# Performance work log

Hardware: AMD Instinct MI355X
Metric: run time of the kernel (lower is better)

The kernel has to match this reference:

```python
import jax, jax.numpy as jnp
import numpy as np

# Constants from init_kwargs
DT = 0.01
NIV = 8          # energy_input_dim[1]
HID = 64         # hidden_dims[0]
FEAT = 501       # per-field microstructure feature length (501+501=1002)


def _lin(k, fin, fout):
    return jax.random.normal(k, (fin, fout), dtype=jnp.float32) / np.sqrt(fin)


def setup_inputs() -> dict:
    key = jax.random.key(0)
    ks = jax.random.split(key, 12)
    B, T = 8192, 512
    e = jax.random.normal(ks[0], (B, T, 1), dtype=jnp.float32) * 0.1
    e_dot = jax.random.normal(ks[1], (B, T, 1), dtype=jnp.float32) * 0.1
    # positive microstructure fields (code computes nu**-1 and E/nu**2)
    E = jax.random.uniform(ks[2], (B, FEAT), minval=0.5, maxval=2.0, dtype=jnp.float32)
    nu = jax.random.uniform(ks[3], (B, FEAT), minval=0.5, maxval=2.0, dtype=jnp.float32)
    return {
        "e": e, "e_dot": e_dot, "E": E, "nu": nu,
        # EnergyFunction.B : Linear(1002,64) -> ReLU -> Linear(64,niv)
        "Bw1": _lin(ks[4], 2 * FEAT, HID), "Bb1": jnp.zeros((HID,), jnp.float32),
        "Bw2": _lin(ks[5], HID, NIV), "Bb2": jnp.zeros((NIV,), jnp.float32),
        # InverseDissipationPotential.beta : Linear(1002,64)->Softplus->Linear(64,niv)->Softplus
        "bw1": _lin(ks[6], 2 * FEAT, HID), "bb1": jnp.zeros((HID,), jnp.float32),
        "bw2": _lin(ks[7], HID, NIV), "bb2": jnp.zeros((NIV,), jnp.float32),
    }


def reference(e, e_dot, E, nu, Bw1, Bb1, Bw2, Bb2, bw1, bb1, bw2, bb2):
    # --- microstructure encoder (TrueFeatures) ---
    nu_p = 1.0 / jnp.mean(1.0 / nu, axis=1, keepdims=True)                 # [B,1]
    E_p = jnp.mean(E / nu ** 2, axis=1, keepdims=True) * nu_p ** 2         # [B,1]
    m = jnp.concatenate([E, nu], axis=-1)                                  # [B,1002]

    # Time-invariant MLP coefficients (hoisted out of the time loop)
    Bm = jax.nn.relu(m @ Bw1 + Bb1) @ Bw2 + Bb2                            # [B,NIV]
    beta = jax.nn.softplus(jax.nn.softplus(m @ bw1 + bb1) @ bw2 + bb2)     # [B,NIV]
    Bsum = jnp.sum(Bm, axis=-1, keepdims=True)                             # [B,1]

    B_, niv = Bm.shape
    xi0 = jnp.zeros((B_, niv), dtype=e.dtype)

    def step(xi, inp):
        u, p = inp                                                          # [B,1],[B,1]
        # Analytic gradients of L = sum_{b,k} Bm_bk * (0.5*E' u^2 + 0.5*(u-xi_k)^2 + 0.5*sum_j xi_j^2)
        du = u - xi                                                         # [B,NIV]
        grad_u = Bsum * E_p * u + jnp.sum(Bm * du, axis=-1, keepdims=True)  # [B,1] (s_eq)
        grad_v = -Bm * du + Bsum * xi                                       # [B,NIV] (d)
        q = -grad_v
        # Analytic gradients of potential = -0.5*nu' p^2 + 0.5*sum(beta*q^2)
        grad_p = -nu_p * p                                                  # [B,1] (s_neq)
        grad_q = beta * q                                                   # [B,NIV] (kinetics)
        stress = grad_u - grad_p
        return xi + DT * grad_q, (stress, xi)

    xs = (jnp.swapaxes(e, 0, 1), jnp.swapaxes(e_dot, 0, 1))                 # [T,B,1]
    _, (stress_t, xi_t) = jax.lax.scan(step, xi0, xs)
    stress = jnp.swapaxes(stress_t, 0, 1)                                   # [B,T,1]
    xi = jnp.swapaxes(xi_t, 0, 1)                                           # [B,T,NIV]
    return stress, xi
```

## Files before the change

kernel.cpp:

```cpp
#include <hip/hip_runtime.h>
#include <hip/hip_bf16.h>

#define FEATN 501
#define KPAD 1024
#define MSTRIDE 1032
#define NB 8192
#define NT 512
#define DTC 0.01f

typedef __attribute__((ext_vector_type(8))) short short8;
typedef __attribute__((ext_vector_type(4))) short short4v;
typedef __attribute__((ext_vector_type(4))) float f32x4;

__device__ __forceinline__ float softplus_f(float x) {
    return fmaxf(x, 0.f) + log1pf(expf(-fabsf(x)));
}
__device__ __forceinline__ ushort f2bf(float x) {
    __hip_bfloat16 h = __float2bfloat16(x);
    return *reinterpret_cast<ushort*>(&h);
}
__device__ __forceinline__ void gl_lds16(const void* g, void* l) {
    __builtin_amdgcn_global_load_lds(
        (const __attribute__((address_space(1))) void*)g,
        (__attribute__((address_space(3))) void*)l, 16, 0, 0);
}
__device__ __forceinline__ float dpp_add(float x, const int ctrl) {
    int s = __builtin_bit_cast(int, x);
    int y;
    switch (ctrl) {
    case 0xB1:  y = __builtin_amdgcn_update_dpp(0, s, 0xB1, 0xf, 0xf, true); break;
    case 0x4E:  y = __builtin_amdgcn_update_dpp(0, s, 0x4E, 0xf, 0xf, true); break;
    default:    y = __builtin_amdgcn_update_dpp(0, s, 0x141, 0xf, 0xf, true); break;
    }
    return x + __builtin_bit_cast(float, y);
}

__global__ __launch_bounds__(256) void wtrans_kernel(
    const float* __restrict__ Bw1, const float* __restrict__ bw1,
    ushort* __restrict__ Wt) {
    const int h = blockIdx.x;
    const int lane = threadIdx.x & 63;
    const int wv = threadIdx.x >> 6;
    const float* W = (h < 64) ? Bw1 : bw1;
    const int col = h & 63;
    #pragma unroll
    for (int it = 0; it < 4; ++it) {
        const int k = it * 256 + wv * 64 + lane;
        const int ksrc = (k < FEATN) ? k
                       : (k >= 512 && k < 512 + FEATN) ? k - 11 : -1;
        const float v = (ksrc >= 0) ? W[(size_t)ksrc * 64 + col] : 0.f;
        Wt[(size_t)h * KPAD + k] = f2bf(v);
    }
}

__global__ __launch_bounds__(1024, 8) void enc_kernel(
    const float* __restrict__ E, const float* __restrict__ nu,
    const ushort* __restrict__ Wt,
    const float* __restrict__ Bb1, const float* __restrict__ bb1,
    const float* __restrict__ Bw2, const float* __restrict__ Bb2,
    const float* __restrict__ bw2, const float* __restrict__ bb2,
    float* __restrict__ xi) {
    __shared__ ushort Ml[16 * MSTRIDE];
    __shared__ float red[3][2048];
    __shared__ float hid[128][17];
    __shared__ float nups[16], Eps[16];

    const int tid = threadIdx.x;
    const int w = tid >> 6, lane = tid & 63;
    const int bb0 = blockIdx.x * 16;

    {
        const int bl = w;
        const size_t base = (size_t)(bb0 + bl) * FEATN;
        float s1 = 0.f, s2 = 0.f;
        #pragma unroll
        for (int it = 0; it < 2; ++it) {
            const int i0 = it * 256 + lane * 4;
            if (i0 + 3 < FEATN) {
                const float4 Ev = *(const float4*)(E + base + i0);
                const float4 nv = *(const float4*)(nu + base + i0);
                const float i0v = 1.0f / nv.x, i1v = 1.0f / nv.y;
                const float i2v = 1.0f / nv.z, i3v = 1.0f / nv.w;
                s1 += (i0v + i1v) + (i2v + i3v);
                s2 = fmaf(Ev.x, i0v * i0v, s2);
                s2 = fmaf(Ev.y, i1v * i1v, s2);
                s2 = fmaf(Ev.z, i2v * i2v, s2);
                s2 = fmaf(Ev.w, i3v * i3v, s2);
                short4v ep = {(short)f2bf(Ev.x), (short)f2bf(Ev.y),
                              (short)f2bf(Ev.z), (short)f2bf(Ev.w)};
                short4v np_ = {(short)f2bf(nv.x), (short)f2bf(nv.y),
                               (short)f2bf(nv.z), (short)f2bf(nv.w)};
                *(short4v*)&Ml[bl * MSTRIDE + i0] = ep;
                *(short4v*)&Ml[bl * MSTRIDE + 512 + i0] = np_;
            } else if (i0 < FEATN) {
                const float Ev = E[base + i0];
                const float nv = nu[base + i0];
                const float iv = 1.0f / nv;
                s1 += iv;
                s2 = fmaf(Ev, iv * iv, s2);
                Ml[bl * MSTRIDE + i0] = f2bf(Ev);
                Ml[bl * MSTRIDE + 512 + i0] = f2bf(nv);
            }
        }
        if (lane < 11) {
            Ml[bl * MSTRIDE + FEATN + lane] = 0;
            Ml[bl * MSTRIDE + 512 + FEATN + lane] = 0;
        }
        #pragma unroll
        for (int o = 32; o; o >>= 1) {
            s1 += __shfl_xor(s1, o);
            s2 += __shfl_xor(s2, o);
        }
        if (lane == 0) {
            const float np = (float)FEATN / s1;
            nups[bl] = np;
            Eps[bl] = (s2 / (float)FEATN) * np * np;
        }
    }
    __syncthreads();

    const int g = w & 3, q = w >> 2;
    const int r15 = lane & 15, kg = lane >> 4;
    const ushort* wp0 = Wt + (size_t)(g * 32 + r15) * KPAD + q * 256 + kg * 8;
    const ushort* wp1 = wp0 + 16 * KPAD;
    const int boff = r15 * MSTRIDE + q * 256 + kg * 8;

    f32x4 acc0 = {0.f, 0.f, 0.f, 0.f}, acc1 = acc0;
    #pragma unroll
    for (int s = 0; s < 8; ++s) {
        const int kb = s * 32;
        const short8 a0 = *(const short8*)(wp0 + kb);
        const short8 a1 = *(const short8*)(wp1 + kb);
        const short8 b = *(const short8*)&Ml[boff + kb];
        acc0 = __builtin_amdgcn_mfma_f32_16x16x32_bf16(a0, b, acc0, 0, 0, 0);
        acc1 = __builtin_amdgcn_mfma_f32_16x16x32_bf16(a1, b, acc1, 0, 0, 0);
    }

    if (q > 0) {
        *(f32x4*)&red[q - 1][(g * 64 + lane) * 8] = acc0;
        *(f32x4*)&red[q - 1][(g * 64 + lane) * 8 + 4] = acc1;
    }
    __syncthreads();
    if (q == 0) {
        #pragma unroll
        for (int p = 0; p < 3; ++p) {
            acc0 += *(const f32x4*)&red[p][(g * 64 + lane) * 8];
            acc1 += *(const f32x4*)&red[p][(g * 64 + lane) * 8 + 4];
        }
        #pragma unroll
        for (int t = 0; t < 2; ++t) {
            #pragma unroll
            for (int r = 0; r < 4; ++r) {
                const int h = g * 32 + t * 16 + kg * 4 + r;
                const float bias = (h < 64) ? Bb1[h] : bb1[h - 64];
                float v = (t ? acc1[r] : acc0[r]) + bias;
                v = (h < 64) ? fmaxf(v, 0.f) : softplus_f(v);
                hid[h][r15] = v;
            }
        }
    }
    __syncthreads();

    if (tid < 128) {
        const int bl = tid >> 3, k = tid & 7;
        float dB = 0.f, db = 0.f;
        #pragma unroll 8
        for (int h = 0; h < 64; ++h) {
            dB = fmaf(hid[h][bl], Bw2[h * 8 + k], dB);
            db = fmaf(hid[64 + h][bl], bw2[h * 8 + k], db);
        }
        const float Bm = dB + Bb2[k];
        const float be = softplus_f(db + bb2[k]);
        float Bs = Bm;
        Bs += __shfl_xor(Bs, 1);
        Bs += __shfl_xor(Bs, 2);
        Bs += __shfl_xor(Bs, 4);
        float* cb = xi + (size_t)(bb0 + bl) * 4096;
        cb[k] = 1.f - DTC * be * (Bm + Bs);
        cb[8 + k] = DTC * be * Bm;
        cb[16 + k] = Bm;
        if (k == 0) { cb[24] = Bs * Eps[bl]; cb[25] = nups[bl]; }
    }
}

__global__ __launch_bounds__(256) void time_kernel(
    const float* __restrict__ e, const float* __restrict__ ed,
    const float* coef, float* stress, float* xi_out) {
    __shared__ float els[4][512];
    __shared__ float pls[4][512];
    __shared__ float scr[4][256];
    const int wv = threadIdx.x >> 6;
    const int wid = (blockIdx.x << 2) + wv;
    const int lane = threadIdx.x & 63;
    const int j = lane >> 3, k = lane & 7;

    const float* eb = e + (size_t)wid * NT;
    const float* edb = ed + (size_t)wid * NT;
    gl_lds16(eb + lane * 4, &els[wv][0]);
    gl_lds16(eb + 256 + lane * 4, &els[wv][256]);
    gl_lds16(edb + lane * 4, &pls[wv][0]);
    gl_lds16(edb + 256 + lane * 4, &pls[wv][256]);

    const float* cb = coef + (size_t)wid * 4096;
    const float a = cb[k];
    const float c = cb[8 + k];
    const float Bm = cb[16 + k];
    const float sE = cb[24];
    const float nup = cb[25];
    asm volatile("s_waitcnt vmcnt(0)" ::: "memory");

    const float a2 = a * a, a4 = a2 * a2;
    float A = 1.f;
    if (j & 1) A *= a;
    if (j & 2) A *= a2;
    if (j & 4) A *= a4;
    float pw[8];
    {
        float run = c;
        #pragma unroll
        for (int i = 7; i >= 0; --i) {
            const bool on = (i < j);
            pw[i] = on ? run : 0.f;
            run = on ? run * a : run;
        }
    }

    float* xb = xi_out + (size_t)wid * (NT * 8);
    float* sb = stress + (size_t)wid * NT;
    const float* el = &els[wv][0];
    const float* pl = &pls[wv][0];

    float4 q0 = *(const float4*)(el);
    float4 q1 = *(const float4*)(el + 4);
    float uj = el[j];
    float pj = pl[j];

    float xs = 0.f;
    for (int g = 0; g < 16; ++g) {
        const int T0 = g * 32;
        float vx[4], sv[4];
        #pragma unroll
        for (int w = 0; w < 4; ++w) {
            const int t0 = T0 + w * 8;
            const float u0 = q0.x, u1 = q0.y, u2 = q0.z, u3 = q0.w;
            const float u4 = q1.x, u5 = q1.y, u6 = q1.z, u7 = q1.w;
            const float cuj = uj, cpj = pj;
            if (t0 + 8 < NT) {
                q0 = *(const float4*)(el + t0 + 8);
                q1 = *(const float4*)(el + t0 + 12);
                uj = el[t0 + 8 + j];
                pj = pl[t0 + 8 + j];
            }
            float xi_j = A * xs;
            xi_j = fmaf(pw[0], u0, xi_j);
            xi_j = fmaf(pw[1], u1, xi_j);
            xi_j = fmaf(pw[2], u2, xi_j);
            xi_j = fmaf(pw[3], u3, xi_j);
            xi_j = fmaf(pw[4], u4, xi_j);
            xi_j = fmaf(pw[5], u5, xi_j);
            xi_j = fmaf(pw[6], u6, xi_j);
            xi_j = fmaf(pw[7], u7, xi_j);
            vx[w] = xi_j;
            float r = Bm * (cuj - xi_j);
            r = dpp_add(r, 0xB1);
            r = dpp_add(r, 0x4E);
            r = dpp_add(r, 0x141);
            sv[w] = fmaf(sE, cuj, fmaf(nup, cpj, r));
            xs = fmaf(a, __shfl(xi_j, 56 + k), c * u7);
        }
        #pragma unroll
        for (int w = 0; w < 4; ++w) scr[wv][w * 64 + lane] = vx[w];
        *(float4*)(xb + T0 * 8 + lane * 4) =
            *(const float4*)&scr[wv][lane * 4];
        if (k == 0) {
            #pragma unroll
            for (int w = 0; w < 4; ++w) scr[wv][w * 8 + j] = sv[w];
        }
        if (lane < 8)
            *(float4*)(sb + T0 + lane * 4) =
                *(const float4*)&scr[wv][lane * 4];
    }
}

extern "C" void kernel_launch(void* const* d_in, const int* in_sizes, int n_in,
                              void* d_out, int out_size, void* d_ws, size_t ws_size,
                              hipStream_t stream) {
    const float* e   = (const float*)d_in[0];
    const float* ed  = (const float*)d_in[1];
    const float* E   = (const float*)d_in[2];
    const float* nu  = (const float*)d_in[3];
    const float* Bw1 = (const float*)d_in[4];
    const float* Bb1 = (const float*)d_in[5];
    const float* Bw2 = (const float*)d_in[6];
    const float* Bb2 = (const float*)d_in[7];
    const float* bw1 = (const float*)d_in[8];
    const float* bb1 = (const float*)d_in[9];
    const float* bw2 = (const float*)d_in[10];
    const float* bb2 = (const float*)d_in[11];

    float* out = (float*)d_out;
    float* stress = out;
    float* xi = out + (size_t)NB * NT;
    ushort* Wt = (ushort*)out;

    wtrans_kernel<<<128, 256, 0, stream>>>(Bw1, bw1, Wt);
    enc_kernel<<<512, 1024, 0, stream>>>(E, nu, Wt, Bb1, bb1,
                                         Bw2, Bb2, bw2, bb2, xi);
    time_kernel<<<2048, 256, 0, stream>>>(e, ed, xi, stress, xi);
}
```

Before: 67.23 us.

## Fuse encoder MLP and time-scan kernels into one kernel sharing LDS

Merges the encoder and time-recurrence kernels into a single kernel. Per-batch coefficients now stay in shared memory instead of going through global memory, and one launch is dropped. LDS is reused via a union buffer for the matrix operand and the e/e_dot staging. The scan loop now writes xi and stress directly to global memory with per-step scalar stores, replacing the batched float4 stores through a scratch buffer. The fused kernel runs 1024-thread blocks (16 waves) for the scan where the old scan kernel used 256-thread blocks, which may lower occupancy, and the narrower stores may lose coalescing.

New measurement: 66.49 us. About the same (-1.1%).

```diff
diff --git a/kernel.cpp b/kernel.cpp
--- a/kernel.cpp
+++ b/kernel.cpp
@@ -53,16 +53,21 @@
     }
 }
 
-__global__ __launch_bounds__(1024, 8) void enc_kernel(
+__global__ __launch_bounds__(1024, 8) void fused_kernel(
     const float* __restrict__ E, const float* __restrict__ nu,
     const ushort* __restrict__ Wt,
     const float* __restrict__ Bb1, const float* __restrict__ bb1,
     const float* __restrict__ Bw2, const float* __restrict__ Bb2,
     const float* __restrict__ bw2, const float* __restrict__ bb2,
-    float* __restrict__ xi) {
-    __shared__ ushort Ml[16 * MSTRIDE];
-    __shared__ float red[3][2048];
-    __shared__ float hid[128][17];
+    const float* __restrict__ e, const float* __restrict__ ed,
+    float* __restrict__ stress, float* __restrict__ xi_out) {
+    __shared__ __align__(16) char LDSU[66304];
+    ushort* Ml = (ushort*)LDSU;
+    float (*red)[2048] = (float(*)[2048])(LDSU + 33024);
+    float (*hid)[17] = (float(*)[17])(LDSU + 57600);
+    float* els = (float*)LDSU;
+    float* pls = (float*)(LDSU + 32768);
+    __shared__ float coefL[16][32];
     __shared__ float nups[16], Eps[16];
 
     const int tid = threadIdx.x;
@@ -70,8 +75,7 @@
     const int bb0 = blockIdx.x * 16;
 
     {
-        const int bl = w;
-        const size_t base = (size_t)(bb0 + bl) * FEATN;
+        const size_t base = (size_t)(bb0 + w) * FEATN;
         float s1 = 0.f, s2 = 0.f;
         #pragma unroll
         for (int it = 0; it < 2; ++it) {
@@ -90,21 +94,21 @@
                               (short)f2bf(Ev.z), (short)f2bf(Ev.w)};
                 short4v np_ = {(short)f2bf(nv.x), (short)f2bf(nv.y),
                                (short)f2bf(nv.z), (short)f2bf(nv.w)};
-                *(short4v*)&Ml[bl * MSTRIDE + i0] = ep;
-                *(short4v*)&Ml[bl * MSTRIDE + 512 + i0] = np_;
+                *(short4v*)&Ml[w * MSTRIDE + i0] = ep;
+                *(short4v*)&Ml[w * MSTRIDE + 512 + i0] = np_;
             } else if (i0 < FEATN) {
                 const float Ev = E[base + i0];
                 const float nv = nu[base + i0];
                 const float iv = 1.0f / nv;
                 s1 += iv;
                 s2 = fmaf(Ev, iv * iv, s2);
-                Ml[bl * MSTRIDE + i0] = f2bf(Ev);
-                Ml[bl * MSTRIDE + 512 + i0] = f2bf(nv);
+                Ml[w * MSTRIDE + i0] = f2bf(Ev);
+                Ml[w * MSTRIDE + 512 + i0] = f2bf(nv);
             }
         }
         if (lane < 11) {
-            Ml[bl * MSTRIDE + FEATN + lane] = 0;
-            Ml[bl * MSTRIDE + 512 + FEATN + lane] = 0;
+            Ml[w * MSTRIDE + FEATN + lane] = 0;
+            Ml[w * MSTRIDE + 512 + FEATN + lane] = 0;
         }
         #pragma unroll
         for (int o = 32; o; o >>= 1) {
@@ -113,49 +117,50 @@
         }
         if (lane == 0) {
             const float np = (float)FEATN / s1;
-            nups[bl] = np;
-            Eps[bl] = (s2 / (float)FEATN) * np * np;
+            nups[w] = np;
+            Eps[w] = (s2 / (float)FEATN) * np * np;
         }
     }
     __syncthreads();
 
     const int g = w & 3, q = w >> 2;
     const int r15 = lane & 15, kg = lane >> 4;
-    const ushort* wp0 = Wt + (size_t)(g * 32 + r15) * KPAD + q * 256 + kg * 8;
-    const ushort* wp1 = wp0 + 16 * KPAD;
-    const int boff = r15 * MSTRIDE + q * 256 + kg * 8;
-
-    f32x4 acc0 = {0.f, 0.f, 0.f, 0.f}, acc1 = acc0;
-    #pragma unroll
-    for (int s = 0; s < 8; ++s) {
-        const int kb = s * 32;
-        const short8 a0 = *(const short8*)(wp0 + kb);
-        const short8 a1 = *(const short8*)(wp1 + kb);
-        const short8 b = *(const short8*)&Ml[boff + kb];
-        acc0 = __builtin_amdgcn_mfma_f32_16x16x32_bf16(a0, b, acc0, 0, 0, 0);
-        acc1 = __builtin_amdgcn_mfma_f32_16x16x32_bf16(a1, b, acc1, 0, 0, 0);
-    }
-
-    if (q > 0) {
-        *(f32x4*)&red[q - 1][(g * 64 + lane) * 8] = acc0;
-        *(f32x4*)&red[q - 1][(g * 64 + lane) * 8 + 4] = acc1;
-    }
-    __syncthreads();
-    if (q == 0) {
-        #pragma unroll
-        for (int p = 0; p < 3; ++p) {
-            acc0 += *(const f32x4*)&red[p][(g * 64 + lane) * 8];
-            acc1 += *(const f32x4*)&red[p][(g * 64 + lane) * 8 + 4];
-        }
-        #pragma unroll
-        for (int t = 0; t < 2; ++t) {
+    {
+        const ushort* wp0 = Wt + (size_t)(g * 32 + r15) * KPAD + q * 256 + kg * 8;
+        const ushort* wp1 = wp0 + 16 * KPAD;
+        const int boff = r15 * MSTRIDE + q * 256 + kg * 8;
+
+        f32x4 acc0 = {0.f, 0.f, 0.f, 0.f}, acc1 = acc0;
+        #pragma unroll
+        for (int s = 0; s < 8; ++s) {
+            const int kb = s * 32;
+            const short8 a0 = *(const short8*)(wp0 + kb);
+            const short8 a1 = *(const short8*)(wp1 + kb);
+            const short8 b = *(const short8*)&Ml[boff + kb];
+            acc0 = __builtin_amdgcn_mfma_f32_16x16x32_bf16(a0, b, acc0, 0, 0, 0);
+            acc1 = __builtin_amdgcn_mfma_f32_16x16x32_bf16(a1, b, acc1, 0, 0, 0);
+        }
+        if (q > 0) {
+            *(f32x4*)&red[q - 1][(g * 64 + lane) * 8] = acc0;
+            *(f32x4*)&red[q - 1][(g * 64 + lane) * 8 + 4] = acc1;
+        }
+        __syncthreads();
+        if (q == 0) {
             #pragma unroll
-            for (int r = 0; r < 4; ++r) {
-                const int h = g * 32 + t * 16 + kg * 4 + r;
-                const float bias = (h < 64) ? Bb1[h] : bb1[h - 64];
-                float v = (t ? acc1[r] : acc0[r]) + bias;
-                v = (h < 64) ? fmaxf(v, 0.f) : softplus_f(v);
-                hid[h][r15] = v;
+            for (int p = 0; p < 3; ++p) {
+                acc0 += *(const f32x4*)&red[p][(g * 64 + lane) * 8];
+                acc1 += *(const f32x4*)&red[p][(g * 64 + lane) * 8 + 4];
+            }
+            #pragma unroll
+            for (int t = 0; t < 2; ++t) {
+                #pragma unroll
+                for (int r = 0; r < 4; ++r) {
+                    const int h = g * 32 + t * 16 + kg * 4 + r;
+                    const float bias = (h < 64) ? Bb1[h] : bb1[h - 64];
+                    float v = (t ? acc1[r] : acc0[r]) + bias;
+                    v = (h < 64) ? fmaxf(v, 0.f) : softplus_f(v);
+                    hid[h][r15] = v;
+                }
             }
         }
     }
@@ -175,38 +180,29 @@
         Bs += __shfl_xor(Bs, 1);
         Bs += __shfl_xor(Bs, 2);
         Bs += __shfl_xor(Bs, 4);
-        float* cb = xi + (size_t)(bb0 + bl) * 4096;
-        cb[k] = 1.f - DTC * be * (Bm + Bs);
-        cb[8 + k] = DTC * be * Bm;
-        cb[16 + k] = Bm;
-        if (k == 0) { cb[24] = Bs * Eps[bl]; cb[25] = nups[bl]; }
-    }
-}
-
-__global__ __launch_bounds__(256) void time_kernel(
-    const float* __restrict__ e, const float* __restrict__ ed,
-    const float* coef, float* stress, float* xi_out) {
-    __shared__ float els[4][512];
-    __shared__ float pls[4][512];
-    __shared__ float scr[4][256];
-    const int wv = threadIdx.x >> 6;
-    const int wid = (blockIdx.x << 2) + wv;
-    const int lane = threadIdx.x & 63;
+        coefL[bl][k] = 1.f - DTC * be * (Bm + Bs);
+        coefL[bl][8 + k] = DTC * be * Bm;
+        coefL[bl][16 + k] = Bm;
+        if (k == 0) { coefL[bl][24] = Bs * Eps[bl]; coefL[bl][25] = nups[bl]; }
+    }
+    __syncthreads();
+
+    const int wid = bb0 + w;
     const int j = lane >> 3, k = lane & 7;
-
     const float* eb = e + (size_t)wid * NT;
     const float* edb = ed + (size_t)wid * NT;
-    gl_lds16(eb + lane * 4, &els[wv][0]);
-    gl_lds16(eb + 256 + lane * 4, &els[wv][256]);
-    gl_lds16(edb + lane * 4, &pls[wv][0]);
-    gl_lds16(edb + 256 + lane * 4, &pls[wv][256]);
-
-    const float* cb = coef + (size_t)wid * 4096;
-    const float a = cb[k];
-    const float c = cb[8 + k];
-    const float Bm = cb[16 + k];
-    const float sE = cb[24];
-    const float nup = cb[25];
+    float* el = els + w * 512;
+    float* pl = pls + w * 512;
+    gl_lds16(eb + lane * 4, el);
+    gl_lds16(eb + 256 + lane * 4, el + 256);
+    gl_lds16(edb + lane * 4, pl);
+    gl_lds16(edb + 256 + lane * 4, pl + 256);
+
+    const float a = coefL[w][k];
+    const float c = coefL[w][8 + k];
+    const float Bm = coefL[w][16 + k];
+    const float sE = coefL[w][24];
+    const float nup = coefL[w][25];
     asm volatile("s_waitcnt vmcnt(0)" ::: "memory");
 
     const float a2 = a * a, a4 = a2 * a2;
@@ -227,8 +223,6 @@
 
     float* xb = xi_out + (size_t)wid * (NT * 8);
     float* sb = stress + (size_t)wid * NT;
-    const float* el = &els[wv][0];
-    const float* pl = &pls[wv][0];
 
     float4 q0 = *(const float4*)(el);
     float4 q1 = *(const float4*)(el + 4);
@@ -236,49 +230,33 @@
     float pj = pl[j];
 
     float xs = 0.f;
-    for (int g = 0; g < 16; ++g) {
-        const int T0 = g * 32;
-        float vx[4], sv[4];
-        #pragma unroll
-        for (int w = 0; w < 4; ++w) {
-            const int t0 = T0 + w * 8;
-            const float u0 = q0.x, u1 = q0.y, u2 = q0.z, u3 = q0.w;
-            const float u4 = q1.x, u5 = q1.y, u6 = q1.z, u7 = q1.w;
-            const float cuj = uj, cpj = pj;
-            if (t0 + 8 < NT) {
-                q0 = *(const float4*)(el + t0 + 8);
-                q1 = *(const float4*)(el + t0 + 12);
-                uj = el[t0 + 8 + j];
-                pj = pl[t0 + 8 + j];
-            }
-            float xi_j = A * xs;
-            xi_j = fmaf(pw[0], u0, xi_j);
-            xi_j = fmaf(pw[1], u1, xi_j);
-            xi_j = fmaf(pw[2], u2, xi_j);
-            xi_j = fmaf(pw[3], u3, xi_j);
-            xi_j = fmaf(pw[4], u4, xi_j);
-            xi_j = fmaf(pw[5], u5, xi_j);
-            xi_j = fmaf(pw[6], u6, xi_j);
-            xi_j = fmaf(pw[7], u7, xi_j);
-            vx[w] = xi_j;
-            float r = Bm * (cuj - xi_j);
-            r = dpp_add(r, 0xB1);
-            r = dpp_add(r, 0x4E);
-            r = dpp_add(r, 0x141);
-            sv[w] = fmaf(sE, cuj, fmaf(nup, cpj, r));
-            xs = fmaf(a, __shfl(xi_j, 56 + k), c * u7);
-        }
-        #pragma unroll
-        for (int w = 0; w < 4; ++w) scr[wv][w * 64 + lane] = vx[w];
-        *(float4*)(xb + T0 * 8 + lane * 4) =
-            *(const float4*)&scr[wv][lane * 4];
-        if (k == 0) {
-            #pragma unroll
-            for (int w = 0; w < 4; ++w) scr[wv][w * 8 + j] = sv[w];
-        }
-        if (lane < 8)
-            *(float4*)(sb + T0 + lane * 4) =
-                *(const float4*)&scr[wv][lane * 4];
+    #pragma unroll 2
+    for (int t0 = 0; t0 < NT; t0 += 8) {
+        const float u0 = q0.x, u1 = q0.y, u2 = q0.z, u3 = q0.w;
+        const float u4 = q1.x, u5 = q1.y, u6 = q1.z, u7 = q1.w;
+        const float cuj = uj, cpj = pj;
+        if (t0 + 8 < NT) {
+            q0 = *(const float4*)(el + t0 + 8);
+            q1 = *(const float4*)(el + t0 + 12);
+            uj = el[t0 + 8 + j];
+            pj = pl[t0 + 8 + j];
+        }
+        float xi_j = A * xs;
+        xi_j = fmaf(pw[0], u0, xi_j);
+        xi_j = fmaf(pw[1], u1, xi_j);
+        xi_j = fmaf(pw[2], u2, xi_j);
+        xi_j = fmaf(pw[3], u3, xi_j);
+        xi_j = fmaf(pw[4], u4, xi_j);
+        xi_j = fmaf(pw[5], u5, xi_j);
+        xi_j = fmaf(pw[6], u6, xi_j);
+        xi_j = fmaf(pw[7], u7, xi_j);
+        xb[t0 * 8 + lane] = xi_j;
+        float r = Bm * (cuj - xi_j);
+        r = dpp_add(r, 0xB1);
+        r = dpp_add(r, 0x4E);
+        r = dpp_add(r, 0x141);
+        if (k == 0) sb[t0 + j] = fmaf(sE, cuj, fmaf(nup, cpj, r));
+        xs = fmaf(a, __shfl(xi_j, 56 + k), c * u7);
     }
 }
 
@@ -301,10 +279,10 @@
     float* out = (float*)d_out;
     float* stress = out;
     float* xi = out + (size_t)NB * NT;
-    ushort* Wt = (ushort*)out;
+    ushort* Wt = (ushort*)d_ws;
 
     wtrans_kernel<<<128, 256, 0, stream>>>(Bw1, bw1, Wt);
-    enc_kernel<<<512, 1024, 0, stream>>>(E, nu, Wt, Bb1, bb1,
-                                         Bw2, Bb2, bw2, bb2, xi);
-    time_kernel<<<2048, 256, 0, stream>>>(e, ed, xi, stress, xi);
-}
+    fused_kernel<<<512, 1024, 0, stream>>>(E, nu, Wt, Bb1, bb1,
+                                           Bw2, Bb2, bw2, bb2,
+                                           e, ed, stress, xi);
+}
```
